# Performance work log

Measured on AMD Instinct MI355X. Metric: run time of the kernel, lower is better.

Reference implementation:

```python
import jax, jax.numpy as jnp
import numpy as np

B, K, T, C = 4, 8, 2048, 64

def setup_inputs() -> dict:
    key = jax.random.key(0)
    ks = jax.random.split(key, 7)
    return {
        "x": jax.random.normal(ks[0], (B, K, T, C), dtype=jnp.float32),
        "Wq": jax.random.normal(ks[1], (C, C), dtype=jnp.float32) / np.sqrt(C),
        "bq": jax.random.normal(ks[2], (C,), dtype=jnp.float32) * 0.01,
        "Wk": jax.random.normal(ks[3], (C, C), dtype=jnp.float32) / np.sqrt(C),
        "bk": jax.random.normal(ks[4], (C,), dtype=jnp.float32) * 0.01,
        "Wv": jax.random.normal(ks[5], (C, C), dtype=jnp.float32) / np.sqrt(C),
        "bv": jax.random.normal(ks[6], (C,), dtype=jnp.float32) * 0.01,
    }

def reference(x, Wq, bq, Wk, bk, Wv, bv):
    c_dim = x.shape[-1]
    # torch nn.Linear: y = x @ W.T + b
    q = jnp.einsum('bktc,dc->bktd', x, Wq) + bq
    k = jnp.einsum('bktc,dc->bktd', x, Wk) + bk
    v = jnp.einsum('bktc,dc->bktd', x, Wv) + bv
    scores = jnp.einsum('bkic,bkjc->bkij', q, k) / jnp.sqrt(jnp.float32(c_dim))
    attn = jax.nn.softmax(scores, axis=-1)
    out = jnp.einsum('bkij,bkjc->bkic', attn, v)
    return out
```

## Files before the change

kernel.cpp:

```cpp
#include <hip/hip_runtime.h>


#define T_DIM 2048
#define NHEAD 32
#define HSTRIDE (T_DIM * 64)
#define QSCALE 0.18033688011112042f
#define SOFF  8.0f

#define SWZ(row, grp) ((row) * 64 + ((((grp) ^ ((row) & 7)) & 7) * 8))

#define RAW_BARRIER() asm volatile("s_waitcnt lgkmcnt(0)\n\ts_barrier" ::: "memory")

typedef _Float16 h8 __attribute__((ext_vector_type(8)));
typedef _Float16 h4 __attribute__((ext_vector_type(4)));
typedef __fp16   g2 __attribute__((ext_vector_type(2)));
typedef float    f4 __attribute__((ext_vector_type(4)));

union H4U { h4 v; g2 p[2]; };
union H8U { h8 v; h4 h[2]; };

#if defined(__has_builtin)
#if __has_builtin(__builtin_amdgcn_exp2f)
#define EXP2(x) __builtin_amdgcn_exp2f(x)
#endif
#endif
#ifndef EXP2
__device__ inline float exp2_raw(float x) {
    float r;
    asm("v_exp_f32 %0, %1" : "=v"(r) : "v"(x));
    return r;
}
#define EXP2(x) exp2_raw(x)
#endif

__device__ inline h4 cvt4(f4 x) {
    H4U u;
    u.p[0] = __builtin_amdgcn_cvt_pkrtz(x[0], x[1]);
    u.p[1] = __builtin_amdgcn_cvt_pkrtz(x[2], x[3]);
    return u.v;
}

__device__ inline h8 cvt8(f4 a, f4 b) {
    H8U r;
    r.h[0] = cvt4(a);
    r.h[1] = cvt4(b);
    return r.v;
}

__global__ __launch_bounds__(256) void qkv_proj_kernel(
    const float* __restrict__ x,
    const float* __restrict__ Wq, const float* __restrict__ bq,
    const float* __restrict__ Wk, const float* __restrict__ bk,
    const float* __restrict__ Wv, const float* __restrict__ bv,
    _Float16* __restrict__ qh, _Float16* __restrict__ khT,
    _Float16* __restrict__ vtT)
{
    __shared__ _Float16 ws[3][64 * 64];
    __shared__ _Float16 ot[64 * 64];
    __shared__ float bsh[3][64];

    const int tid  = threadIdx.x;
    const int row0 = blockIdx.x * 64;
    const int head = blockIdx.x >> 5;
    const int t0   = (blockIdx.x & 31) * 64;

    #pragma unroll
    for (int m = 0; m < 3; ++m) {
        const float* Wm = (m == 0) ? Wq : ((m == 1) ? Wk : Wv);
        const float* bm = (m == 0) ? bq : ((m == 1) ? bk : bv);
        #pragma unroll
        for (int pass = 0; pass < 4; ++pass) {
            const int idx = pass * 1024 + tid * 4;
            const int d = idx >> 6, c = idx & 63;
            f4 wv = *(const f4*)(Wm + idx);
            *(h4*)&ws[m][SWZ(d, c >> 3) + (c & 7)] = cvt4(wv);
        }
        if (tid < 64) bsh[m][tid] = bm[tid];
    }

    const int w    = tid >> 6;
    const int lane = tid & 63;
    const int l15  = lane & 15;
    const int qd   = lane >> 4;

    h8 af[2];
    {
        const float* xp = x + (size_t)(row0 + w * 16 + l15) * 64 + qd * 8;
        #pragma unroll
        for (int ch = 0; ch < 2; ++ch) {
            f4 a0 = *(const f4*)(xp + ch * 32);
            f4 a1 = *(const f4*)(xp + ch * 32 + 4);
            af[ch] = cvt8(a0, a1);
        }
    }
    __syncthreads();

    #pragma unroll
    for (int m = 0; m < 3; ++m) {
        h8 bf[4][2];
        #pragma unroll
        for (int ns = 0; ns < 4; ++ns)
            #pragma unroll
            for (int ch = 0; ch < 2; ++ch)
                bf[ns][ch] = *(const h8*)&ws[m][SWZ(ns * 16 + l15, ch * 4 + qd)];

        f4 acc[4];
        #pragma unroll
        for (int ns = 0; ns < 4; ++ns)
            acc[ns] = (f4){0.f, 0.f, 0.f, 0.f};
        #pragma unroll
        for (int ch = 0; ch < 2; ++ch)
            #pragma unroll
            for (int ns = 0; ns < 4; ++ns)
                acc[ns] = __builtin_amdgcn_mfma_f32_16x16x32_f16(
                    af[ch], bf[ns][ch], acc[ns], 0, 0, 0);

        __syncthreads();
        if (m < 2) {
            #pragma unroll
            for (int ns = 0; ns < 4; ++ns) {
                const int d = ns * 16 + l15;
                const float bias = bsh[m][d];
                #pragma unroll
                for (int r = 0; r < 4; ++r) {
                    const int t = w * 16 + qd * 4 + r;
                    float v = acc[ns][r] + bias;
                    if (m == 0) v *= QSCALE;
                    ot[SWZ(t, d >> 3) + (d & 7)] = (_Float16)v;
                }
            }
            __syncthreads();
            if (m == 0) {
                #pragma unroll
                for (int pass = 0; pass < 2; ++pass) {
                    const int t  = pass * 32 + (tid >> 3);
                    const int c0 = (tid & 7) * 8;
                    *(h8*)&qh[(size_t)(row0 + t) * 64 + c0] =
                        *(const h8*)&ot[SWZ(t, tid & 7)];
                }
            } else {
                #pragma unroll
                for (int pass = 0; pass < 2; ++pass) {
                    const int f    = pass * 2048 + tid * 8;
                    const int Jl   = f >> 10;
                    const int rest = f & 1023;
                    const int ch_  = rest >> 9;
                    const int qd_  = (rest >> 7) & 3;
                    const int l15_ = (rest >> 3) & 15;
                    h8 val = *(const h8*)&ot[SWZ(Jl * 16 + l15_, ch_ * 4 + qd_)];
                    *(h8*)&khT[(size_t)head * HSTRIDE + ((t0 >> 4) + Jl) * 1024 + rest] = val;
                }
            }
        } else {
            #pragma unroll
            for (int ns = 0; ns < 4; ++ns) {
                const int d = ns * 16 + l15;
                const float bias = bsh[2][d];
                const int tl = w * 16 + qd * 4;
                f4 pvf;
                #pragma unroll
                for (int r = 0; r < 4; ++r)
                    pvf[r] = acc[ns][r] + bias;
                *(h4*)&ot[SWZ(d, tl >> 3) + (tl & 7)] = cvt4(pvf);
            }
            __syncthreads();
            #pragma unroll
            for (int pass = 0; pass < 2; ++pass) {
                const int f   = pass * 2048 + tid * 8;
                const int qd3 = f >> 10;
                const int rem = f & 1023;
                const int c   = rem >> 4;
                const int g   = (rem & 15) >> 3;
                const int ta  = (2 * g) * 16 + qd3 * 4;
                const int tb  = ta + 16;
                H8U val;
                val.h[0] = *(const h4*)&ot[SWZ(c, ta >> 3) + (ta & 7)];
                val.h[1] = *(const h4*)&ot[SWZ(c, tb >> 3) + (tb & 7)];
                *(h8*)&vtT[(size_t)head * HSTRIDE + (t0 >> 6) * 4096 + f] = val.v;
            }
        }
    }
}

__global__ __launch_bounds__(384) void attn_kernel(
    const _Float16* __restrict__ qh, const _Float16* __restrict__ khT,
    const _Float16* __restrict__ vtT, float* __restrict__ out)
{
    __shared__ _Float16 tiles[2][8192];
    const int tid  = threadIdx.x;
    const int w    = tid >> 6;
    const int lane = tid & 63;
    const int l15  = lane & 15;
    const int qd   = lane >> 4;

    const int bid  = blockIdx.x;
    const int xcd  = bid & 7;
    const int slot = bid >> 3;
    const int head = xcd * 4 + (slot >> 4);
    const int qpart = slot & 15;

    if (w < 4) {
        const int q0 = qpart * 128 + w * 32;

        h8 qf[2][2];
        #pragma unroll
        for (int is = 0; is < 2; ++is) {
            const _Float16* qp = qh + (size_t)(head * T_DIM + q0 + is * 16 + l15) * 64 + qd * 8;
            qf[is][0] = *(const h8*)qp;
            qf[is][1] = *(const h8*)(qp + 32);
        }

        f4 rs4[2] = {(f4){0.f,0.f,0.f,0.f}, (f4){0.f,0.f,0.f,0.f}};
        f4 oacc[2][4];
        #pragma unroll
        for (int is = 0; is < 2; ++is)
            #pragma unroll
            for (int cs = 0; cs < 4; ++cs)
                oacc[is][cs] = (f4){0.f, 0.f, 0.f, 0.f};

        const int ko = lane * 8;
        __syncthreads();

        for (int it = 0; it < 32; ++it) {
            const _Float16* kb = &tiles[it & 1][0];
            const _Float16* vb = kb + 4096;

            h8 kf[4][2];
            #pragma unroll
            for (int jt = 0; jt < 4; ++jt)
                #pragma unroll
                for (int ch = 0; ch < 2; ++ch)
                    kf[jt][ch] = *(const h8*)(kb + jt * 1024 + ch * 512 + ko);
            H8U vf8[4][2];
            #pragma unroll
            for (int cs = 0; cs < 4; ++cs) {
                vf8[cs][0].v = *(const h8*)(vb + (cs * 2 + 0) * 512 + ko);
                vf8[cs][1].v = *(const h8*)(vb + (cs * 2 + 1) * 512 + ko);
            }

            f4 st[4][2];
            #pragma unroll
            for (int jt = 0; jt < 4; ++jt)
                #pragma unroll
                for (int is = 0; is < 2; ++is)
                    st[jt][is] = (f4){-SOFF, -SOFF, -SOFF, -SOFF};
            #pragma unroll
            for (int ch = 0; ch < 2; ++ch)
                #pragma unroll
                for (int jt = 0; jt < 4; ++jt)
                    #pragma unroll
                    for (int is = 0; is < 2; ++is)
                        st[jt][is] = __builtin_amdgcn_mfma_f32_16x16x32_f16(
                            kf[jt][ch], qf[is][ch], st[jt][is], 0, 0, 0);

            h4 pf[4][2];
            #pragma unroll
            for (int is = 0; is < 2; ++is)
                #pragma unroll
                for (int jt = 0; jt < 4; ++jt) {
                    f4 p;
                    p[0] = EXP2(st[jt][is][0]);
                    p[1] = EXP2(st[jt][is][1]);
                    p[2] = EXP2(st[jt][is][2]);
                    p[3] = EXP2(st[jt][is][3]);
                    rs4[is] += p;
                    pf[jt][is] = cvt4(p);
                }

            #pragma unroll
            for (int jt = 0; jt < 4; ++jt)
                #pragma unroll
                for (int cs = 0; cs < 4; ++cs)
                    #pragma unroll
                    for (int is = 0; is < 2; ++is)
                        oacc[is][cs] = __builtin_amdgcn_mfma_f32_16x16x16f16(
                            pf[jt][is], vf8[cs][jt >> 1].h[jt & 1], oacc[is][cs], 0, 0, 0);

            __syncthreads();
        }

        #pragma unroll
        for (int is = 0; is < 2; ++is) {
            float l = (rs4[is][0] + rs4[is][1]) + (rs4[is][2] + rs4[is][3]);
            l += __shfl_xor(l, 16, 64);
            l += __shfl_xor(l, 32, 64);
            const float linvv = 1.f / l;
            float linv[4];
            #pragma unroll
            for (int r = 0; r < 4; ++r)
                linv[r] = __shfl(linvv, qd * 4 + r, 64);
            #pragma unroll
            for (int cs = 0; cs < 4; ++cs) {
                const int c = cs * 16 + l15;
                #pragma unroll
                for (int r = 0; r < 4; ++r) {
                    const int t = q0 + is * 16 + qd * 4 + r;
                    out[(size_t)(head * T_DIM + t) * 64 + c] = oacc[is][cs][r] * linv[r];
                }
            }
        }
    } else if (w == 4) {
        const _Float16* kT = khT + (size_t)head * HSTRIDE;
        const int lo = lane * 8;
        h8 sA[8], sB[8];
        #pragma unroll
        for (int b = 0; b < 8; ++b) sA[b] = *(const h8*)(kT + b * 512 + lo);
        #pragma unroll
        for (int b = 0; b < 8; ++b) sB[b] = *(const h8*)(kT + 4096 + b * 512 + lo);
        const _Float16* kp = kT + 8192;
        #pragma unroll
        for (int b = 0; b < 8; ++b) *(h8*)(&tiles[0][0] + b * 512 + lo) = sA[b];
        RAW_BARRIER();

        for (int it2 = 0; it2 < 16; ++it2) {
            if (it2 < 15) {
                #pragma unroll
                for (int b = 0; b < 8; ++b) sA[b] = *(const h8*)(kp + b * 512 + lo);
                kp += 4096;
            }
            #pragma unroll
            for (int b = 0; b < 8; ++b) *(h8*)(&tiles[1][0] + b * 512 + lo) = sB[b];
            RAW_BARRIER();
            if (it2 < 15) {
                #pragma unroll
                for (int b = 0; b < 8; ++b) sB[b] = *(const h8*)(kp + b * 512 + lo);
                kp += 4096;
                #pragma unroll
                for (int b = 0; b < 8; ++b) *(h8*)(&tiles[0][0] + b * 512 + lo) = sA[b];
            }
            RAW_BARRIER();
        }
    } else {
        const _Float16* vT = vtT + (size_t)head * HSTRIDE;
        const int lo  = lane * 8;
        const int voA = (lane >> 4) * 1024 + (lane & 15) * 16;
        h8 sA[8], sB[8];
        #pragma unroll
        for (int b = 0; b < 8; ++b)
            sA[b] = *(const h8*)(vT + voA + (b >> 1) * 256 + (b & 1) * 8);
        #pragma unroll
        for (int b = 0; b < 8; ++b)
            sB[b] = *(const h8*)(vT + 4096 + voA + (b >> 1) * 256 + (b & 1) * 8);
        const _Float16* vp = vT + 8192;
        #pragma unroll
        for (int b = 0; b < 8; ++b) *(h8*)(&tiles[0][4096] + b * 512 + lo) = sA[b];
        RAW_BARRIER();

        for (int it2 = 0; it2 < 16; ++it2) {
            if (it2 < 15) {
                #pragma unroll
                for (int b = 0; b < 8; ++b)
                    sA[b] = *(const h8*)(vp + voA + (b >> 1) * 256 + (b & 1) * 8);
                vp += 4096;
            }
            #pragma unroll
            for (int b = 0; b < 8; ++b) *(h8*)(&tiles[1][4096] + b * 512 + lo) = sB[b];
            RAW_BARRIER();
            if (it2 < 15) {
                #pragma unroll
                for (int b = 0; b < 8; ++b)
                    sB[b] = *(const h8*)(vp + voA + (b >> 1) * 256 + (b & 1) * 8);
                vp += 4096;
                #pragma unroll
                for (int b = 0; b < 8; ++b) *(h8*)(&tiles[0][4096] + b * 512 + lo) = sA[b];
            }
            RAW_BARRIER();
        }
    }
}

extern "C" void kernel_launch(void* const* d_in, const int* in_sizes, int n_in,
                              void* d_out, int out_size, void* d_ws, size_t ws_size,
                              hipStream_t stream)
{
    (void)in_sizes; (void)n_in; (void)out_size; (void)ws_size;
    const float* x  = (const float*)d_in[0];
    const float* Wq = (const float*)d_in[1];
    const float* bq = (const float*)d_in[2];
    const float* Wk = (const float*)d_in[3];
    const float* bk = (const float*)d_in[4];
    const float* Wv = (const float*)d_in[5];
    const float* bv = (const float*)d_in[6];
    float* out = (float*)d_out;

    _Float16* qh  = (_Float16*)d_ws;
    _Float16* khT = qh + (size_t)NHEAD * HSTRIDE;
    _Float16* vtT = khT + (size_t)NHEAD * HSTRIDE;

    hipLaunchKernelGGL(qkv_proj_kernel, dim3(1024), dim3(256), 0, stream,
                       x, Wq, bq, Wk, bk, Wv, bv, qh, khT, vtT);
    hipLaunchKernelGGL(attn_kernel, dim3(512), dim3(384), 0, stream,
                       qh, khT, vtT, out);
}
```

Before: 128.6 us.

## Switch attention MFMAs to 32x32x16 tiles and re-layout K/V workspace

The attention inner loop now uses 32x32x16 f16 MFMA instructions for both QK^T and PV instead of 16x16 variants, with Q fragments, softmax packing and output indexing rewritten for the 32x32 register layout. The projection kernel writes K and V into a new pre-swizzled order so the loader waves can copy contiguous chunks with one shared code path. Launch bounds now request 3 blocks per CU. The aim is fewer MFMA issues and fewer fragment loads per tile. The cost is more accumulator registers, which may pressure occupancy.

```diff
diff --git a/kernel.cpp b/kernel.cpp
--- a/kernel.cpp
+++ b/kernel.cpp
@@ -15,9 +15,10 @@
 typedef _Float16 h4 __attribute__((ext_vector_type(4)));
 typedef __fp16   g2 __attribute__((ext_vector_type(2)));
 typedef float    f4 __attribute__((ext_vector_type(4)));
+typedef float    fv16 __attribute__((ext_vector_type(16)));
 
 union H4U { h4 v; g2 p[2]; };
-union H8U { h8 v; h4 h[2]; };
+union H8U { h8 v; h4 h[2]; g2 p[4]; };
 
 #if defined(__has_builtin)
 #if __has_builtin(__builtin_amdgcn_exp2f)
@@ -45,6 +46,13 @@
     r.h[0] = cvt4(a);
     r.h[1] = cvt4(b);
     return r.v;
+}
+
+__device__ inline fv16 splat16(float x) {
+    fv16 r;
+    #pragma unroll
+    for (int i = 0; i < 16; ++i) r[i] = x;
+    return r;
 }
 
 __global__ __launch_bounds__(256) void qkv_proj_kernel(
@@ -141,14 +149,18 @@
             } else {
                 #pragma unroll
                 for (int pass = 0; pass < 2; ++pass) {
-                    const int f    = pass * 2048 + tid * 8;
-                    const int Jl   = f >> 10;
-                    const int rest = f & 1023;
-                    const int ch_  = rest >> 9;
-                    const int qd_  = (rest >> 7) & 3;
-                    const int l15_ = (rest >> 3) & 15;
-                    h8 val = *(const h8*)&ot[SWZ(Jl * 16 + l15_, ch_ * 4 + qd_)];
-                    *(h8*)&khT[(size_t)head * HSTRIDE + ((t0 >> 4) + Jl) * 1024 + rest] = val;
+                    const int f   = pass * 2048 + tid * 8;
+                    const int kb  = f >> 11;
+                    const int cs  = (f >> 9) & 3;
+                    const int l   = (f >> 3) & 63;
+                    const int p   = l & 31;
+                    const int w16 = p & 15;
+                    const int sw  = ((w16 & 12) == 4) ? (w16 + 4)
+                                  : (((w16 & 12) == 8) ? (w16 - 4) : w16);
+                    const int tact = kb * 32 + (p & 16) + sw;
+                    const int g8   = cs * 2 + (l >> 5);
+                    *(h8*)&khT[(size_t)head * HSTRIDE + (t0 >> 6) * 4096 + f] =
+                        *(const h8*)&ot[SWZ(tact, g8)];
                 }
             }
         } else {
@@ -166,23 +178,20 @@
             __syncthreads();
             #pragma unroll
             for (int pass = 0; pass < 2; ++pass) {
-                const int f   = pass * 2048 + tid * 8;
-                const int qd3 = f >> 10;
-                const int rem = f & 1023;
-                const int c   = rem >> 4;
-                const int g   = (rem & 15) >> 3;
-                const int ta  = (2 * g) * 16 + qd3 * 4;
-                const int tb  = ta + 16;
-                H8U val;
-                val.h[0] = *(const h4*)&ot[SWZ(c, ta >> 3) + (ta & 7)];
-                val.h[1] = *(const h4*)&ot[SWZ(c, tb >> 3) + (tb & 7)];
-                *(h8*)&vtT[(size_t)head * HSTRIDE + (t0 >> 6) * 4096 + f] = val.v;
+                const int f  = pass * 2048 + tid * 8;
+                const int q2 = f >> 9;
+                const int b  = q2 >> 1, cc = q2 & 1;
+                const int l  = (f >> 3) & 63;
+                const int c  = cc * 32 + (l & 31);
+                const int tg = b * 2 + (l >> 5);
+                *(h8*)&vtT[(size_t)head * HSTRIDE + (t0 >> 6) * 4096 + f] =
+                    *(const h8*)&ot[SWZ(c, tg)];
             }
         }
     }
 }
 
-__global__ __launch_bounds__(384) void attn_kernel(
+__global__ __launch_bounds__(384, 3) void attn_kernel(
     const _Float16* __restrict__ qh, const _Float16* __restrict__ khT,
     const _Float16* __restrict__ vtT, float* __restrict__ out)
 {
@@ -190,8 +199,6 @@
     const int tid  = threadIdx.x;
     const int w    = tid >> 6;
     const int lane = tid & 63;
-    const int l15  = lane & 15;
-    const int qd   = lane >> 4;
 
     const int bid  = blockIdx.x;
     const int xcd  = bid & 7;
@@ -200,169 +207,119 @@
     const int qpart = slot & 15;
 
     if (w < 4) {
-        const int q0 = qpart * 128 + w * 32;
-
-        h8 qf[2][2];
-        #pragma unroll
-        for (int is = 0; is < 2; ++is) {
-            const _Float16* qp = qh + (size_t)(head * T_DIM + q0 + is * 16 + l15) * 64 + qd * 8;
-            qf[is][0] = *(const h8*)qp;
-            qf[is][1] = *(const h8*)(qp + 32);
-        }
-
-        f4 rs4[2] = {(f4){0.f,0.f,0.f,0.f}, (f4){0.f,0.f,0.f,0.f}};
-        f4 oacc[2][4];
-        #pragma unroll
-        for (int is = 0; is < 2; ++is)
+        const int q0  = qpart * 128 + w * 32;
+        const int l31 = lane & 31;
+        const int lh  = lane >> 5;
+
+        h8 qf[4];
+        {
+            const _Float16* qp = qh + (size_t)(head * T_DIM + q0 + l31) * 64 + lh * 8;
             #pragma unroll
             for (int cs = 0; cs < 4; ++cs)
-                oacc[is][cs] = (f4){0.f, 0.f, 0.f, 0.f};
+                qf[cs] = *(const h8*)(qp + cs * 16);
+        }
+
+        f4 rs4 = (f4){0.f, 0.f, 0.f, 0.f};
+        fv16 oacc[2];
+        oacc[0] = splat16(0.f);
+        oacc[1] = splat16(0.f);
 
         const int ko = lane * 8;
         __syncthreads();
 
         for (int it = 0; it < 32; ++it) {
-            const _Float16* kb = &tiles[it & 1][0];
-            const _Float16* vb = kb + 4096;
-
-            h8 kf[4][2];
-            #pragma unroll
-            for (int jt = 0; jt < 4; ++jt)
-                #pragma unroll
-                for (int ch = 0; ch < 2; ++ch)
-                    kf[jt][ch] = *(const h8*)(kb + jt * 1024 + ch * 512 + ko);
-            H8U vf8[4][2];
-            #pragma unroll
-            for (int cs = 0; cs < 4; ++cs) {
-                vf8[cs][0].v = *(const h8*)(vb + (cs * 2 + 0) * 512 + ko);
-                vf8[cs][1].v = *(const h8*)(vb + (cs * 2 + 1) * 512 + ko);
-            }
-
-            f4 st[4][2];
-            #pragma unroll
-            for (int jt = 0; jt < 4; ++jt)
-                #pragma unroll
-                for (int is = 0; is < 2; ++is)
-                    st[jt][is] = (f4){-SOFF, -SOFF, -SOFF, -SOFF};
-            #pragma unroll
-            for (int ch = 0; ch < 2; ++ch)
-                #pragma unroll
-                for (int jt = 0; jt < 4; ++jt)
-                    #pragma unroll
-                    for (int is = 0; is < 2; ++is)
-                        st[jt][is] = __builtin_amdgcn_mfma_f32_16x16x32_f16(
-                            kf[jt][ch], qf[is][ch], st[jt][is], 0, 0, 0);
-
-            h4 pf[4][2];
-            #pragma unroll
-            for (int is = 0; is < 2; ++is)
-                #pragma unroll
-                for (int jt = 0; jt < 4; ++jt) {
+            const _Float16* kb_ = &tiles[it & 1][0];
+            const _Float16* vb_ = kb_ + 4096;
+
+            fv16 st[2];
+            #pragma unroll
+            for (int kb = 0; kb < 2; ++kb) {
+                h8 kf[4];
+                #pragma unroll
+                for (int cs = 0; cs < 4; ++cs)
+                    kf[cs] = *(const h8*)(kb_ + kb * 2048 + cs * 512 + ko);
+                st[kb] = splat16(-SOFF);
+                #pragma unroll
+                for (int cs = 0; cs < 4; ++cs)
+                    st[kb] = __builtin_amdgcn_mfma_f32_32x32x16_f16(
+                        kf[cs], qf[cs], st[kb], 0, 0, 0);
+            }
+
+            h8 vf[4][2];
+            #pragma unroll
+            for (int b = 0; b < 4; ++b)
+                #pragma unroll
+                for (int cc = 0; cc < 2; ++cc)
+                    vf[b][cc] = *(const h8*)(vb_ + (b * 2 + cc) * 512 + ko);
+
+            H8U pa[4];
+            #pragma unroll
+            for (int kb = 0; kb < 2; ++kb)
+                #pragma unroll
+                for (int g = 0; g < 4; ++g) {
                     f4 p;
-                    p[0] = EXP2(st[jt][is][0]);
-                    p[1] = EXP2(st[jt][is][1]);
-                    p[2] = EXP2(st[jt][is][2]);
-                    p[3] = EXP2(st[jt][is][3]);
-                    rs4[is] += p;
-                    pf[jt][is] = cvt4(p);
+                    p[0] = EXP2(st[kb][4 * g + 0]);
+                    p[1] = EXP2(st[kb][4 * g + 1]);
+                    p[2] = EXP2(st[kb][4 * g + 2]);
+                    p[3] = EXP2(st[kb][4 * g + 3]);
+                    rs4 += p;
+                    const int b = kb * 2 + (g >> 1);
+                    pa[b].p[(g & 1) * 2 + 0] = __builtin_amdgcn_cvt_pkrtz(p[0], p[1]);
+                    pa[b].p[(g & 1) * 2 + 1] = __builtin_amdgcn_cvt_pkrtz(p[2], p[3]);
                 }
 
             #pragma unroll
-            for (int jt = 0; jt < 4; ++jt)
-                #pragma unroll
-                for (int cs = 0; cs < 4; ++cs)
-                    #pragma unroll
-                    for (int is = 0; is < 2; ++is)
-                        oacc[is][cs] = __builtin_amdgcn_mfma_f32_16x16x16f16(
-                            pf[jt][is], vf8[cs][jt >> 1].h[jt & 1], oacc[is][cs], 0, 0, 0);
+            for (int b = 0; b < 4; ++b)
+                #pragma unroll
+                for (int cc = 0; cc < 2; ++cc)
+                    oacc[cc] = __builtin_amdgcn_mfma_f32_32x32x16_f16(
+                        pa[b].v, vf[b][cc], oacc[cc], 0, 0, 0);
 
             __syncthreads();
         }
 
-        #pragma unroll
-        for (int is = 0; is < 2; ++is) {
-            float l = (rs4[is][0] + rs4[is][1]) + (rs4[is][2] + rs4[is][3]);
-            l += __shfl_xor(l, 16, 64);
-            l += __shfl_xor(l, 32, 64);
-            const float linvv = 1.f / l;
-            float linv[4];
-            #pragma unroll
-            for (int r = 0; r < 4; ++r)
-                linv[r] = __shfl(linvv, qd * 4 + r, 64);
-            #pragma unroll
-            for (int cs = 0; cs < 4; ++cs) {
-                const int c = cs * 16 + l15;
-                #pragma unroll
-                for (int r = 0; r < 4; ++r) {
-                    const int t = q0 + is * 16 + qd * 4 + r;
-                    out[(size_t)(head * T_DIM + t) * 64 + c] = oacc[is][cs][r] * linv[r];
-                }
-            }
-        }
-    } else if (w == 4) {
-        const _Float16* kT = khT + (size_t)head * HSTRIDE;
+        float lsum = (rs4[0] + rs4[1]) + (rs4[2] + rs4[3]);
+        lsum += __shfl_xor(lsum, 32, 64);
+        const float linv = 1.f / lsum;
+        #pragma unroll
+        for (int r = 0; r < 16; ++r) {
+            const int qrow = (r & 3) + 8 * (r >> 2) + 4 * lh;
+            const float fac = __shfl(linv, qrow, 64);
+            #pragma unroll
+            for (int cc = 0; cc < 2; ++cc)
+                out[(size_t)(head * T_DIM + q0 + qrow) * 64 + cc * 32 + l31] =
+                    oacc[cc][r] * fac;
+        }
+    } else {
+        const _Float16* src = ((w == 4) ? khT : vtT) + (size_t)head * HSTRIDE;
+        _Float16* d0 = &tiles[0][(w - 4) * 4096];
+        _Float16* d1 = &tiles[1][(w - 4) * 4096];
         const int lo = lane * 8;
         h8 sA[8], sB[8];
         #pragma unroll
-        for (int b = 0; b < 8; ++b) sA[b] = *(const h8*)(kT + b * 512 + lo);
-        #pragma unroll
-        for (int b = 0; b < 8; ++b) sB[b] = *(const h8*)(kT + 4096 + b * 512 + lo);
-        const _Float16* kp = kT + 8192;
-        #pragma unroll
-        for (int b = 0; b < 8; ++b) *(h8*)(&tiles[0][0] + b * 512 + lo) = sA[b];
+        for (int b = 0; b < 8; ++b) sA[b] = *(const h8*)(src + b * 512 + lo);
+        #pragma unroll
+        for (int b = 0; b < 8; ++b) sB[b] = *(const h8*)(src + 4096 + b * 512 + lo);
+        const _Float16* sp = src + 8192;
+        #pragma unroll
+        for (int b = 0; b < 8; ++b) *(h8*)(d0 + b * 512 + lo) = sA[b];
         RAW_BARRIER();
 
         for (int it2 = 0; it2 < 16; ++it2) {
             if (it2 < 15) {
                 #pragma unroll
-                for (int b = 0; b < 8; ++b) sA[b] = *(const h8*)(kp + b * 512 + lo);
-                kp += 4096;
-            }
-            #pragma unroll
-            for (int b = 0; b < 8; ++b) *(h8*)(&tiles[1][0] + b * 512 + lo) = sB[b];
+                for (int b = 0; b < 8; ++b) sA[b] = *(const h8*)(sp + b * 512 + lo);
+                sp += 4096;
+            }
+            #pragma unroll
+            for (int b = 0; b < 8; ++b) *(h8*)(d1 + b * 512 + lo) = sB[b];
             RAW_BARRIER();
             if (it2 < 15) {
                 #pragma unroll
-                for (int b = 0; b < 8; ++b) sB[b] = *(const h8*)(kp + b * 512 + lo);
-                kp += 4096;
-                #pragma unroll
-                for (int b = 0; b < 8; ++b) *(h8*)(&tiles[0][0] + b * 512 + lo) = sA[b];
-            }
-            RAW_BARRIER();
-        }
-    } else {
-        const _Float16* vT = vtT + (size_t)head * HSTRIDE;
-        const int lo  = lane * 8;
-        const int voA = (lane >> 4) * 1024 + (lane & 15) * 16;
-        h8 sA[8], sB[8];
-        #pragma unroll
-        for (int b = 0; b < 8; ++b)
-            sA[b] = *(const h8*)(vT + voA + (b >> 1) * 256 + (b & 1) * 8);
-        #pragma unroll
-        for (int b = 0; b < 8; ++b)
-            sB[b] = *(const h8*)(vT + 4096 + voA + (b >> 1) * 256 + (b & 1) * 8);
-        const _Float16* vp = vT + 8192;
-        #pragma unroll
-        for (int b = 0; b < 8; ++b) *(h8*)(&tiles[0][4096] + b * 512 + lo) = sA[b];
-        RAW_BARRIER();
-
-        for (int it2 = 0; it2 < 16; ++it2) {
-            if (it2 < 15) {
-                #pragma unroll
-                for (int b = 0; b < 8; ++b)
-                    sA[b] = *(const h8*)(vp + voA + (b >> 1) * 256 + (b & 1) * 8);
-                vp += 4096;
-            }
-            #pragma unroll
-            for (int b = 0; b < 8; ++b) *(h8*)(&tiles[1][4096] + b * 512 + lo) = sB[b];
-            RAW_BARRIER();
-            if (it2 < 15) {
-                #pragma unroll
-                for (int b = 0; b < 8; ++b)
-                    sB[b] = *(const h8*)(vp + voA + (b >> 1) * 256 + (b & 1) * 8);
-                vp += 4096;
-                #pragma unroll
-                for (int b = 0; b < 8; ++b) *(h8*)(&tiles[0][4096] + b * 512 + lo) = sA[b];
+                for (int b = 0; b < 8; ++b) sB[b] = *(const h8*)(sp + b * 512 + lo);
+                sp += 4096;
+                #pragma unroll
+                for (int b = 0; b < 8; ++b) *(h8*)(d0 + b * 512 + lo) = sA[b];
             }
             RAW_BARRIER();
         }
```

Result: no change. 127.9 us (-0.5%).
